# Optimization experiments

Measured on AMD Instinct MI355X. Metric: run time of the kernel, lower is better.

## Reference

```python
import jax, jax.numpy as jnp
import numpy as np

NUM_HEADS = 12
D = 768
HD = D // NUM_HEADS  # 64

def setup_inputs() -> dict:
    key = jax.random.key(0)
    ks = jax.random.split(key, 9)
    s = 0.02
    return {
        "x": jax.random.normal(ks[0], (4, 2048, D), dtype=jnp.float32),
        "QW_w": jax.random.normal(ks[1], (D, D), dtype=jnp.float32) * s,
        "QW_b": jax.random.normal(ks[2], (D,), dtype=jnp.float32) * s,
        "KW_w": jax.random.normal(ks[3], (D, D), dtype=jnp.float32) * s,
        "KW_b": jax.random.normal(ks[4], (D,), dtype=jnp.float32) * s,
        "VW_w": jax.random.normal(ks[5], (D, D), dtype=jnp.float32) * s,
        "VW_b": jax.random.normal(ks[6], (D,), dtype=jnp.float32) * s,
        "OW_w": jax.random.normal(ks[7], (D, D), dtype=jnp.float32) * s,
        "OW_b": jax.random.normal(ks[8], (D,), dtype=jnp.float32) * s,
    }

def reference(x, QW_w, QW_b, KW_w, KW_b, VW_w, VW_b, OW_w, OW_b):
    b, s, _ = x.shape
    # torch nn.Linear: y = x @ W.T + b
    def proj(w, bias):
        y = jnp.einsum('bsd,ed->bse', x, w) + bias
        return y.reshape(b, s, NUM_HEADS, HD).transpose(0, 2, 1, 3)  # [b,h,s,hd]
    q = proj(QW_w, QW_b)
    k = proj(KW_w, KW_b)
    v = proj(VW_w, VW_b)
    scores = jnp.einsum('bhqd,bhkd->bhqk', q, k) / jnp.sqrt(jnp.float32(HD))
    attn = jax.nn.softmax(scores, axis=-1)
    out = jnp.einsum('bhqk,bhkd->bhqd', attn, v)
    out = out.transpose(0, 2, 1, 3).reshape(b, s, NUM_HEADS * HD)
    return jnp.einsum('bsd,ed->bse', out, OW_w) + OW_b
```

## Files before the change

kernel.cpp:

```cpp
#include <hip/hip_runtime.h>
#include <hip/hip_bf16.h>

#define NH  12
#define HD  64
#define DIM 768
#define SEQ 2048
#define NB  4
#define MM  (NB*SEQ)
#define NKB (SEQ/64)

typedef short    v8s  __attribute__((ext_vector_type(8)));
typedef float    v4f  __attribute__((ext_vector_type(4)));
typedef float    v16f __attribute__((ext_vector_type(16)));
typedef unsigned v4u  __attribute__((ext_vector_type(4)));

#if __has_builtin(__builtin_amdgcn_exp2f)
#define EXP2(x) __builtin_amdgcn_exp2f(x)
#else
#define EXP2(x) __builtin_exp2f(x)
#endif

static __device__ __forceinline__ unsigned short f2b(float f) {
    unsigned int u = __float_as_uint(f);
    return (unsigned short)((u + 0x7FFFu + ((u >> 16) & 1u)) >> 16);
}
static __device__ __forceinline__ unsigned cvtpk(float lo, float hi) {
    unsigned r;
    asm("v_cvt_pk_bf16_f32 %0, %1, %2" : "=v"(r) : "v"(lo), "v"(hi));
    return r;
}
static __device__ __forceinline__ void g2l16(const unsigned short* g, unsigned short* l) {
    __builtin_amdgcn_global_load_lds(
        (const __attribute__((address_space(1))) void*)g,
        (__attribute__((address_space(3))) void*)l, 16, 0, 0);
}

__global__ void cast_f32_bf16(const float* __restrict__ in,
                              unsigned short* __restrict__ out, int n4) {
    int i = blockIdx.x * blockDim.x + threadIdx.x;
    if (i < n4) {
        float4 v = reinterpret_cast<const float4*>(in)[i];
        ushort4 o;
        o.x = f2b(v.x); o.y = f2b(v.y); o.z = f2b(v.z); o.w = f2b(v.w);
        reinterpret_cast<ushort4*>(out)[i] = o;
    }
}

__global__ void cast4_f32_bf16(const float* __restrict__ i0, const float* __restrict__ i1,
                               const float* __restrict__ i2, const float* __restrict__ i3,
                               unsigned short* __restrict__ o0, unsigned short* __restrict__ o1,
                               unsigned short* __restrict__ o2, unsigned short* __restrict__ o3,
                               int n4) {
    int i = blockIdx.x * blockDim.x + threadIdx.x;
    if (i >= n4) return;
    const float* in; unsigned short* out;
    switch (blockIdx.y) {
        case 0: in = i0; out = o0; break;
        case 1: in = i1; out = o1; break;
        case 2: in = i2; out = o2; break;
        default: in = i3; out = o3; break;
    }
    float4 v = reinterpret_cast<const float4*>(in)[i];
    ushort4 o;
    o.x = f2b(v.x); o.y = f2b(v.y); o.z = f2b(v.z); o.w = f2b(v.w);
    reinterpret_cast<ushort4*>(out)[i] = o;
}

__global__ __launch_bounds__(256, 3) void gemm_qkv(
    const unsigned short* __restrict__ A,
    const unsigned short* __restrict__ Wq,
    const unsigned short* __restrict__ Wk,
    const unsigned short* __restrict__ Wv,
    const float* __restrict__ bq,
    const float* __restrict__ bk,
    const float* __restrict__ bvp,
    unsigned short* __restrict__ Qb,
    unsigned short* __restrict__ Kfo,
    unsigned short* __restrict__ Vf)
{
    __shared__ __align__(16) unsigned short As[128 * 64];
    __shared__ __align__(16) unsigned short Bs[3][64 * 64];

    const int tid  = threadIdx.x;
    const int w    = tid >> 6, lane = tid & 63;
    const int quad = lane >> 4, l16 = lane & 15;
    const int wm   = w & 1,  wn = w >> 1;
    const int lane8 = lane >> 3, sc = lane & 7;
    const int m0   = blockIdx.x * 128;
    const int h    = blockIdx.y;
    const int n0   = h * 64;

    v4f acc[3][4][2];
    #pragma unroll
    for (int s = 0; s < 3; ++s)
        #pragma unroll
        for (int i = 0; i < 4; ++i)
            #pragma unroll
            for (int j = 0; j < 2; ++j)
                acc[s][i][j] = v4f{0.f, 0.f, 0.f, 0.f};

    for (int kb = 0; kb < DIM; kb += 64) {
        __syncthreads();
        #pragma unroll
        for (int t = 0; t < 4; ++t) {
            int r8 = w * 32 + t * 8;
            int r  = r8 + lane8;
            int gch = sc ^ (r & 7);
            g2l16(&A[(size_t)(m0 + r) * DIM + kb + gch * 8], &As[r8 * 64]);
        }
        #pragma unroll
        for (int u = 0; u < 6; ++u) {
            int G = w * 6 + u;
            int set = G >> 3, rg = G & 7;
            int row = rg * 8 + lane8;
            int gch = sc ^ (row & 7);
            const unsigned short* Wp = (set == 0) ? Wq : (set == 1) ? Wk : Wv;
            g2l16(&Wp[(size_t)(n0 + row) * DIM + kb + gch * 8], &Bs[set][rg * 8 * 64]);
        }
        __syncthreads();
        #pragma unroll
        for (int kk = 0; kk < 64; kk += 32) {
            int chb = kk >> 3;
            v8s a[4];
            #pragma unroll
            for (int i = 0; i < 4; ++i) {
                int m = wm * 64 + i * 16 + l16;
                a[i] = *reinterpret_cast<const v8s*>(
                    &As[m * 64 + (((chb + quad) ^ (m & 7)) << 3)]);
            }
            #pragma unroll
            for (int s = 0; s < 3; ++s) {
                v8s b[2];
                #pragma unroll
                for (int j = 0; j < 2; ++j) {
                    int n = wn * 32 + j * 16 + l16;
                    b[j] = *reinterpret_cast<const v8s*>(
                        &Bs[s][n * 64 + (((chb + quad) ^ (n & 7)) << 3)]);
                }
                #pragma unroll
                for (int i = 0; i < 4; ++i)
                    #pragma unroll
                    for (int j = 0; j < 2; ++j)
                        acc[s][i][j] = __builtin_amdgcn_mfma_f32_16x16x32_bf16(
                            a[i], b[j], acc[s][i][j], 0, 0, 0);
            }
        }
    }

    #pragma unroll
    for (int i = 0; i < 4; ++i) {
        #pragma unroll
        for (int j = 0; j < 2; ++j) {
            int hd = wn * 32 + j * 16 + l16;
            float bias_v = bq[n0 + hd];
            #pragma unroll
            for (int r = 0; r < 4; ++r) {
                int gm = m0 + wm * 64 + i * 16 + quad * 4 + r;
                int bb = gm >> 11, sq = gm & (SEQ - 1);
                Qb[((size_t)(bb * NH + h) * SEQ + sq) * HD + hd] =
                    f2b((acc[0][i][j][r] + bias_v) * 0.1803368801f);
            }
        }
    }
    #pragma unroll
    for (int i = 0; i < 4; ++i) {
        int kh = i >> 1;
        #pragma unroll
        for (int j = 0; j < 2; ++j) {
            int hd = wn * 32 + j * 16 + l16;
            int c  = hd >> 4;
            int half_a = (l16 >> 3) & 1;
            int jj = l16 & 7;
            float bias_v = bk[n0 + hd];
            int gm0 = m0 + wm * 64 + i * 16 + quad * 4;
            int bb = gm0 >> 11, sk = gm0 & (SEQ - 1);
            int t = sk >> 6;
            int l31k = (i & 1) * 16 + quad * 4;
            size_t frag = ((size_t)(bb * NH + h) * NKB + t) * 8 + kh * 4 + c;
            unsigned short* dst = &Kfo[frag * 512 + (half_a * 32 + l31k) * 8 + jj];
            #pragma unroll
            for (int r = 0; r < 4; ++r)
                dst[r * 8] = f2b(acc[1][i][j][r] + bias_v);
        }
    }
    #pragma unroll
    for (int i = 0; i < 4; ++i) {
        #pragma unroll
        for (int j = 0; j < 2; ++j) {
            int hd = wn * 32 + j * 16 + l16;
            int hb = hd >> 5, l31v = hd & 31;
            float bias_v = bvp[n0 + hd];
            int gm0 = m0 + wm * 64 + i * 16 + quad * 4;
            int bb = gm0 >> 11, sk = gm0 & (SEQ - 1);
            int kbi = sk >> 6;
            int halfv = quad >> 1, j0 = (quad & 1) * 4;
            ushort4 pkv;
            pkv.x = f2b(acc[2][i][j][0] + bias_v);
            pkv.y = f2b(acc[2][i][j][1] + bias_v);
            pkv.z = f2b(acc[2][i][j][2] + bias_v);
            pkv.w = f2b(acc[2][i][j][3] + bias_v);
            size_t frag = ((size_t)(bb * NH + h) * NKB + kbi) * 8 + hb * 4 + i;
            *reinterpret_cast<ushort4*>(
                &Vf[frag * 512 + (halfv * 32 + l31v) * 8 + j0]) = pkv;
        }
    }
}

__global__ __launch_bounds__(256, 3) void gemm_o(
    const unsigned short* __restrict__ A,
    const unsigned short* __restrict__ W,
    const float* __restrict__ bias,
    float* __restrict__ out)
{
    __shared__ __align__(16) unsigned short As[128 * 64];
    __shared__ __align__(16) unsigned short Bs[64 * 64];

    const int tid  = threadIdx.x;
    const int w    = tid >> 6, lane = tid & 63;
    const int quad = lane >> 4, l16 = lane & 15;
    const int wm   = w & 1,  wn = w >> 1;
    const int lane8 = lane >> 3, sc = lane & 7;
    const int m0  = blockIdx.x * 128;
    const int n0l = blockIdx.y * 64;

    v4f acc[4][2];
    #pragma unroll
    for (int i = 0; i < 4; ++i)
        #pragma unroll
        for (int j = 0; j < 2; ++j)
            acc[i][j] = v4f{0.f, 0.f, 0.f, 0.f};

    for (int kb = 0; kb < DIM; kb += 64) {
        __syncthreads();
        #pragma unroll
        for (int t = 0; t < 4; ++t) {
            int r8 = w * 32 + t * 8;
            int r  = r8 + lane8;
            int gch = sc ^ (r & 7);
            g2l16(&A[(size_t)(m0 + r) * DIM + kb + gch * 8], &As[r8 * 64]);
        }
        #pragma unroll
        for (int t = 0; t < 2; ++t) {
            int r8 = (w * 2 + t) * 8;
            int r  = r8 + lane8;
            int gch = sc ^ (r & 7);
            g2l16(&W[(size_t)(n0l + r) * DIM + kb + gch * 8], &Bs[r8 * 64]);
        }
        __syncthreads();
        #pragma unroll
        for (int kk = 0; kk < 64; kk += 32) {
            v8s a[4], b[2];
            int chb = kk >> 3;
            #pragma unroll
            for (int i = 0; i < 4; ++i) {
                int m = wm * 64 + i * 16 + l16;
                a[i] = *reinterpret_cast<const v8s*>(
                    &As[m * 64 + (((chb + quad) ^ (m & 7)) << 3)]);
            }
            #pragma unroll
            for (int j = 0; j < 2; ++j) {
                int n = wn * 32 + j * 16 + l16;
                b[j] = *reinterpret_cast<const v8s*>(
                    &Bs[n * 64 + (((chb + quad) ^ (n & 7)) << 3)]);
            }
            #pragma unroll
            for (int i = 0; i < 4; ++i)
                #pragma unroll
                for (int j = 0; j < 2; ++j)
                    acc[i][j] = __builtin_amdgcn_mfma_f32_16x16x32_bf16(a[i], b[j], acc[i][j], 0, 0, 0);
        }
    }

    #pragma unroll
    for (int i = 0; i < 4; ++i) {
        #pragma unroll
        for (int j = 0; j < 2; ++j) {
            int gn = n0l + wn * 32 + j * 16 + l16;
            float bias_v = bias[gn];
            #pragma unroll
            for (int r = 0; r < 4; ++r) {
                int gm = m0 + wm * 64 + i * 16 + quad * 4 + r;
                out[(size_t)gm * DIM + gn] = acc[i][j][r] + bias_v;
            }
        }
    }
}

__global__ __launch_bounds__(256, 3) void attn(
    const unsigned short* __restrict__ Q,
    const unsigned short* __restrict__ Kf,
    const unsigned short* __restrict__ Vf,
    unsigned short* __restrict__ ctx)
{
    __shared__ __align__(16) unsigned short Ks[2][8 * 512];
    __shared__ __align__(16) unsigned short Vs[2][8 * 512];

    const int tid  = threadIdx.x;
    const int w    = tid >> 6, lane = tid & 63;
    const int l31  = lane & 31, half = lane >> 5;

    const int lblk = blockIdx.y * 16 + blockIdx.x;
    const int vblk = (lblk & 7) * 96 + (lblk >> 3);
    const int bh   = vblk >> 4;
    const int b    = bh / NH, h = bh % NH;
    const int q0   = (vblk & 15) * 128 + w * 32;

    const unsigned short* Qp = Q  + ((size_t)bh * SEQ + q0) * HD;
    const unsigned short* Kh = Kf + (size_t)bh * (NKB * 8 * 512);
    const unsigned short* Vh = Vf + (size_t)bh * (NKB * 8 * 512);

    v8s bq[4];
    #pragma unroll
    for (int c = 0; c < 4; ++c)
        bq[c] = *reinterpret_cast<const v8s*>(&Qp[l31 * HD + c * 16 + half * 8]);

    #define STAGE(it_, buf_)                                                   \
        do {                                                                   \
            _Pragma("unroll")                                                  \
            for (int t = 0; t < 2; ++t) {                                      \
                int g = w * 2 + t;                                             \
                g2l16(&Kh[((size_t)(it_) * 8 + g) * 512 + lane * 8],           \
                      &Ks[buf_][g * 512]);                                     \
                g2l16(&Vh[((size_t)(it_) * 8 + g) * 512 + lane * 8],           \
                      &Vs[buf_][g * 512]);                                     \
            }                                                                  \
        } while (0)

    STAGE(0, 0);

    v16f o0a, o0b, o1a, o1b, Z;
    #pragma unroll
    for (int i = 0; i < 16; ++i) {
        o0a[i] = 0.f; o0b[i] = 0.f; o1a[i] = 0.f; o1b[i] = 0.f; Z[i] = 0.f;
    }
    float li = 0.f;

    int cur = 0;
    for (int it = 0; it < NKB; ++it) {
        __syncthreads();
        if (it + 1 < NKB) STAGE(it + 1, cur ^ 1);

        const unsigned short* Kb_ = Ks[cur];
        const unsigned short* Vb_ = Vs[cur];

        v16f s0, s1;
        {
            v8s k0 = *reinterpret_cast<const v8s*>(&Kb_[lane * 8]);
            v8s k1 = *reinterpret_cast<const v8s*>(&Kb_[4 * 512 + lane * 8]);
            s0 = __builtin_amdgcn_mfma_f32_32x32x16_bf16(k0, bq[0], Z, 0, 0, 0);
            s1 = __builtin_amdgcn_mfma_f32_32x32x16_bf16(k1, bq[0], Z, 0, 0, 0);
            #pragma unroll
            for (int c = 1; c < 4; ++c) {
                v8s kc0 = *reinterpret_cast<const v8s*>(&Kb_[(size_t)c * 512 + lane * 8]);
                v8s kc1 = *reinterpret_cast<const v8s*>(&Kb_[(size_t)(4 + c) * 512 + lane * 8]);
                s0 = __builtin_amdgcn_mfma_f32_32x32x16_bf16(kc0, bq[c], s0, 0, 0, 0);
                s1 = __builtin_amdgcn_mfma_f32_32x32x16_bf16(kc1, bq[c], s1, 0, 0, 0);
            }
        }

        unsigned pk[8][2];
        #pragma unroll
        for (int g = 0; g < 4; ++g) {
            float e0 = EXP2(s0[4*g+0]), e1 = EXP2(s0[4*g+1]);
            float e2 = EXP2(s0[4*g+2]), e3 = EXP2(s0[4*g+3]);
            li += (e0 + e1) + (e2 + e3);
            pk[g][0] = cvtpk(e0, e1);
            pk[g][1] = cvtpk(e2, e3);
            float f0 = EXP2(s1[4*g+0]), f1 = EXP2(s1[4*g+1]);
            float f2 = EXP2(s1[4*g+2]), f3 = EXP2(s1[4*g+3]);
            li += (f0 + f1) + (f2 + f3);
            pk[4+g][0] = cvtpk(f0, f1);
            pk[4+g][1] = cvtpk(f2, f3);
        }

        #pragma unroll
        for (int cp = 0; cp < 4; ++cp) {
            unsigned a0 = pk[2*cp][0],   a1 = pk[2*cp][1];
            unsigned b0 = pk[2*cp+1][0], b1 = pk[2*cp+1][1];
            asm("v_permlane32_swap_b32 %0, %1" : "+v"(a0), "+v"(b0));
            asm("v_permlane32_swap_b32 %0, %1" : "+v"(a1), "+v"(b1));
            v4u fw;
            fw.x = a0; fw.y = a1; fw.z = b0; fw.w = b1;
            v8s pf = __builtin_bit_cast(v8s, fw);
            v8s v0 = *reinterpret_cast<const v8s*>(&Vb_[(size_t)cp * 512 + lane * 8]);
            v8s v1 = *reinterpret_cast<const v8s*>(&Vb_[(size_t)(4 + cp) * 512 + lane * 8]);
            if (cp < 2) {
                o0a = __builtin_amdgcn_mfma_f32_32x32x16_bf16(v0, pf, o0a, 0, 0, 0);
                o1a = __builtin_amdgcn_mfma_f32_32x32x16_bf16(v1, pf, o1a, 0, 0, 0);
            } else {
                o0b = __builtin_amdgcn_mfma_f32_32x32x16_bf16(v0, pf, o0b, 0, 0, 0);
                o1b = __builtin_amdgcn_mfma_f32_32x32x16_bf16(v1, pf, o1b, 0, 0, 0);
            }
        }

        cur ^= 1;
    }
    #undef STAGE

    float inv = 1.0f / (li + __shfl_xor(li, 32));

    const int q = q0 + l31;
    size_t base = ((size_t)(b * SEQ + q)) * DIM + h * HD;
    #pragma unroll
    for (int g = 0; g < 4; ++g) {
        int hd0 = 8 * g + 4 * half;
        uint2 u0, u1;
        u0.x = cvtpk((o0a[4*g+0] + o0b[4*g+0]) * inv, (o0a[4*g+1] + o0b[4*g+1]) * inv);
        u0.y = cvtpk((o0a[4*g+2] + o0b[4*g+2]) * inv, (o0a[4*g+3] + o0b[4*g+3]) * inv);
        u1.x = cvtpk((o1a[4*g+0] + o1b[4*g+0]) * inv, (o1a[4*g+1] + o1b[4*g+1]) * inv);
        u1.y = cvtpk((o1a[4*g+2] + o1b[4*g+2]) * inv, (o1a[4*g+3] + o1b[4*g+3]) * inv);
        *reinterpret_cast<uint2*>(&ctx[base + hd0])      = u0;
        *reinterpret_cast<uint2*>(&ctx[base + 32 + hd0]) = u1;
    }
}

extern "C" void kernel_launch(void* const* d_in, const int* in_sizes, int n_in,
                              void* d_out, int out_size, void* d_ws, size_t ws_size,
                              hipStream_t stream) {
    const float* x  = (const float*)d_in[0];
    const float* qw = (const float*)d_in[1]; const float* qb = (const float*)d_in[2];
    const float* kw = (const float*)d_in[3]; const float* kb = (const float*)d_in[4];
    const float* vw = (const float*)d_in[5]; const float* vb = (const float*)d_in[6];
    const float* ow = (const float*)d_in[7]; const float* ob = (const float*)d_in[8];
    float* out = (float*)d_out;

    char* ws = (char*)d_ws;
    size_t off = 0;
    auto alloc = [&](size_t bytes) -> unsigned short* {
        unsigned short* p = (unsigned short*)(ws + off);
        off += (bytes + 255) & ~(size_t)255;
        return p;
    };
    const size_t XB = (size_t)MM * DIM * 2;
    const size_t WB = (size_t)DIM * DIM * 2;
    const size_t QB = (size_t)NB * NH * SEQ * HD * 2;

    unsigned short* xb  = alloc(XB);
    unsigned short* wqb = alloc(WB);
    unsigned short* wkb = alloc(WB);
    unsigned short* wvb = alloc(WB);
    unsigned short* wob = alloc(WB);
    unsigned short* Qb  = alloc(QB);
    unsigned short* Kfb = alloc(QB);
    unsigned short* Vfb = alloc(QB);
    unsigned short* ctx = alloc(XB);

    const int n4x = MM * DIM / 4;
    const int n4w = DIM * DIM / 4;
    cast_f32_bf16<<<(n4x + 255) / 256, 256, 0, stream>>>(x, xb, n4x);
    cast4_f32_bf16<<<dim3((n4w + 255) / 256, 4), 256, 0, stream>>>(
        qw, kw, vw, ow, wqb, wkb, wvb, wob, n4w);

    gemm_qkv<<<dim3(MM / 128, NH), 256, 0, stream>>>(
        xb, wqb, wkb, wvb, qb, kb, vb, Qb, Kfb, Vfb);

    attn<<<dim3(SEQ / 128, NB * NH), 256, 0, stream>>>(Qb, Kfb, Vfb, ctx);

    gemm_o<<<dim3(MM / 128, DIM / 64), 256, 0, stream>>>(ctx, wob, ob, out);
}
```

Measured before the change: 205.3 us.

## Triple-buffer K/V tiles and software-pipeline QK^T one block ahead

```diff
diff --git a/kernel.cpp b/kernel.cpp
--- a/kernel.cpp
+++ b/kernel.cpp
@@ -292,8 +292,8 @@
     const unsigned short* __restrict__ Vf,
     unsigned short* __restrict__ ctx)
 {
-    __shared__ __align__(16) unsigned short Ks[2][8 * 512];
-    __shared__ __align__(16) unsigned short Vs[2][8 * 512];
+    __shared__ __align__(16) unsigned short Ks[3][8 * 512];
+    __shared__ __align__(16) unsigned short Vs[3][8 * 512];
 
     const int tid  = threadIdx.x;
     const int w    = tid >> 6, lane = tid & 63;
@@ -326,7 +326,23 @@
             }                                                                  \
         } while (0)
 
-    STAGE(0, 0);
+    #define QKT(kb_, d0, d1)                                                   \
+        do {                                                                   \
+            const unsigned short* Kb_ = Ks[kb_];                               \
+            v8s k0 = *reinterpret_cast<const v8s*>(&Kb_[lane * 8]);            \
+            v8s k1 = *reinterpret_cast<const v8s*>(&Kb_[4 * 512 + lane * 8]);  \
+            d0 = __builtin_amdgcn_mfma_f32_32x32x16_bf16(k0, bq[0], Z, 0, 0, 0); \
+            d1 = __builtin_amdgcn_mfma_f32_32x32x16_bf16(k1, bq[0], Z, 0, 0, 0); \
+            _Pragma("unroll")                                                  \
+            for (int c = 1; c < 4; ++c) {                                      \
+                v8s kc0 = *reinterpret_cast<const v8s*>(                       \
+                    &Kb_[(size_t)c * 512 + lane * 8]);                         \
+                v8s kc1 = *reinterpret_cast<const v8s*>(                       \
+                    &Kb_[(size_t)(4 + c) * 512 + lane * 8]);                   \
+                d0 = __builtin_amdgcn_mfma_f32_32x32x16_bf16(kc0, bq[c], d0, 0, 0, 0); \
+                d1 = __builtin_amdgcn_mfma_f32_32x32x16_bf16(kc1, bq[c], d1, 0, 0, 0); \
+            }                                                                  \
+        } while (0)
 
     v16f o0a, o0b, o1a, o1b, Z;
     #pragma unroll
@@ -335,29 +351,13 @@
     }
     float li = 0.f;
 
-    int cur = 0;
+    STAGE(0, 0);
+    STAGE(1, 1);
+    __syncthreads();
+    v16f s0, s1;
+    QKT(0, s0, s1);
+
     for (int it = 0; it < NKB; ++it) {
-        __syncthreads();
-        if (it + 1 < NKB) STAGE(it + 1, cur ^ 1);
-
-        const unsigned short* Kb_ = Ks[cur];
-        const unsigned short* Vb_ = Vs[cur];
-
-        v16f s0, s1;
-        {
-            v8s k0 = *reinterpret_cast<const v8s*>(&Kb_[lane * 8]);
-            v8s k1 = *reinterpret_cast<const v8s*>(&Kb_[4 * 512 + lane * 8]);
-            s0 = __builtin_amdgcn_mfma_f32_32x32x16_bf16(k0, bq[0], Z, 0, 0, 0);
-            s1 = __builtin_amdgcn_mfma_f32_32x32x16_bf16(k1, bq[0], Z, 0, 0, 0);
-            #pragma unroll
-            for (int c = 1; c < 4; ++c) {
-                v8s kc0 = *reinterpret_cast<const v8s*>(&Kb_[(size_t)c * 512 + lane * 8]);
-                v8s kc1 = *reinterpret_cast<const v8s*>(&Kb_[(size_t)(4 + c) * 512 + lane * 8]);
-                s0 = __builtin_amdgcn_mfma_f32_32x32x16_bf16(kc0, bq[c], s0, 0, 0, 0);
-                s1 = __builtin_amdgcn_mfma_f32_32x32x16_bf16(kc1, bq[c], s1, 0, 0, 0);
-            }
-        }
-
         unsigned pk[8][2];
         #pragma unroll
         for (int g = 0; g < 4; ++g) {
@@ -373,6 +373,15 @@
             pk[4+g][1] = cvtpk(f2, f3);
         }
 
+        __syncthreads();
+
+        if (it + 2 < NKB) STAGE(it + 2, (it + 2) % 3);
+
+        v16f ns0, ns1;
+        bool more = (it + 1 < NKB);
+        if (more) QKT((it + 1) % 3, ns0, ns1);
+
+        const unsigned short* Vb_ = Vs[it % 3];
         #pragma unroll
         for (int cp = 0; cp < 4; ++cp) {
             unsigned a0 = pk[2*cp][0],   a1 = pk[2*cp][1];
@@ -393,8 +402,9 @@
             }
         }
 
-        cur ^= 1;
-    }
+        if (more) { s0 = ns0; s1 = ns1; }
+    }
+    #undef QKT
     #undef STAGE
 
     float inv = 1.0f / (li + __shfl_xor(li, 32));
```

Result: no change. 207.0 us (+0.8%).
